# Kernel optimization log

Hardware: AMD Instinct MI355X
Metric: run time of the kernel (lower is better)

The kernel has to match this reference:

```python
import jax, jax.numpy as jnp
import numpy as np

N = 20000   # nodes
E = 40000   # directed edges
F_IN = 13   # dataset.num_features
G = 1000    # graphs in batch
DIMS = [(13, 32), (32, 64), (64, 64)]  # (M_in, M_out) per NNConv layer


def setup_inputs() -> dict:
    key = jax.random.key(0)
    ks = list(jax.random.split(key, 32))
    inp = {}
    inp["x"] = jax.random.normal(ks[0], (N, F_IN), jnp.float32)
    inp["edge_index"] = jax.random.randint(ks[1], (2, E), 0, N, dtype=jnp.int32)
    inp["edge_attr"] = jax.random.uniform(ks[2], (E, 5), dtype=jnp.float32)
    inp["batch"] = jnp.sort(jax.random.randint(ks[3], (N,), 0, G, dtype=jnp.int32))
    i = 4
    for l, (mi, mo) in enumerate(DIMS):
        inp[f"w1_{l}"] = jax.random.normal(ks[i], (5, 128), jnp.float32) / np.sqrt(5.0).astype(np.float32); i += 1
        inp[f"b1_{l}"] = jnp.zeros((128,), jnp.float32)
        inp[f"w2_{l}"] = jax.random.normal(ks[i], (128, mi * mo), jnp.float32) / np.sqrt(128.0).astype(np.float32); i += 1
        inp[f"b2_{l}"] = jnp.zeros((mi * mo,), jnp.float32)
        inp[f"root_{l}"] = jax.random.normal(ks[i], (mi, mo), jnp.float32) / np.sqrt(float(mi)).astype(np.float32); i += 1
        inp[f"bias_{l}"] = jnp.zeros((mo,), jnp.float32)
    inp["fc1_w"] = jax.random.normal(ks[i], (64, 32), jnp.float32) / 8.0; i += 1
    inp["fc1_b"] = jnp.zeros((32,), jnp.float32)
    inp["fc2_w"] = jax.random.normal(ks[i], (32, 16), jnp.float32) / np.sqrt(32.0).astype(np.float32); i += 1
    inp["fc2_b"] = jnp.zeros((16,), jnp.float32)
    inp["fc3_w"] = jax.random.normal(ks[i], (16, 1), jnp.float32) / 4.0; i += 1
    inp["fc3_b"] = jnp.zeros((1,), jnp.float32)
    return inp


def _nnconv(x, src, dst, edge_attr, w1, b1, w2, b2, root, bias, mi, mo):
    # edge MLP: [E,5] -> [E,128] -> [E, mi*mo] per-edge weight matrices
    h = jax.nn.relu(edge_attr @ w1 + b1)
    We = (h @ w2 + b2).reshape(-1, mi, mo)          # [E, mi, mo]
    msg = jnp.einsum('ei,eio->eo', x[src], We)      # gather + per-edge matmul
    agg = jax.ops.segment_sum(msg, dst, num_segments=x.shape[0])  # scatter-add
    return x @ root + agg + bias                    # NNConv root weight + bias


def _forward(x, edge_index, edge_attr, batch, convs, fc1_w, fc1_b, fc2_w, fc2_b, fc3_w, fc3_b):
    src, dst = edge_index[0], edge_index[1]
    for (mi, mo), (w1, b1, w2, b2, root, bias) in zip(DIMS, convs):
        x = jax.nn.elu(_nnconv(x, src, dst, edge_attr, w1, b1, w2, b2, root, bias, mi, mo))
    # scatter_mean pooling over graphs
    sums = jax.ops.segment_sum(x, batch, num_segments=G)
    cnt = jax.ops.segment_sum(jnp.ones((x.shape[0],), x.dtype), batch, num_segments=G)
    xg = sums / jnp.maximum(cnt, 1.0)[:, None]
    xg = jax.nn.elu(xg @ fc1_w + fc1_b)
    xg = jax.nn.elu(xg @ fc2_w + fc2_b)
    return (xg @ fc3_w + fc3_b).reshape(-1)


def reference(x, edge_index, edge_attr, batch,
              w1_0, b1_0, w2_0, b2_0, root_0, bias_0,
              w1_1, b1_1, w2_1, b2_1, root_1, bias_1,
              w1_2, b1_2, w2_2, b2_2, root_2, bias_2,
              fc1_w, fc1_b, fc2_w, fc2_b, fc3_w, fc3_b):
    convs = [(w1_0, b1_0, w2_0, b2_0, root_0, bias_0),
             (w1_1, b1_1, w2_1, b2_1, root_1, bias_1),
             (w1_2, b1_2, w2_2, b2_2, root_2, bias_2)]
    return _forward(x, edge_index, edge_attr, batch, convs,
                    fc1_w, fc1_b, fc2_w, fc2_b, fc3_w, fc3_b)
```

## Files before the change

kernel.cpp:

```cpp
#include <hip/hip_runtime.h>
#include <stdint.h>
#include <math.h>

typedef _Float16 half8_t __attribute__((ext_vector_type(8)));
typedef float floatx4 __attribute__((ext_vector_type(4)));

#define NN 20000
#define NE 40000
#define NG 1000
#define NBLK 157
#define NSPLIT 4

__global__ __launch_bounds__(256) void prep_all_kernel(
    const float* __restrict__ w2a, const float* __restrict__ b2a, _Float16* __restrict__ oa,
    const float* __restrict__ w2b, const float* __restrict__ b2b, _Float16* __restrict__ ob,
    const float* __restrict__ w2c, const float* __restrict__ b2c, _Float16* __restrict__ oc)
{
  const int TOT0 = 68 * 2 * 64, TOT1 = 132 * 4 * 64, TOT2 = 264 * 4 * 64;
  int idx = blockIdx.x * 256 + threadIdx.x;
  const float *w2, *b2; _Float16* op; int mi, mo, mpsh, CT;
  if (idx < TOT0) { w2 = w2a; b2 = b2a; op = oa; mi = 13; mo = 32; mpsh = 4; CT = 2; }
  else if (idx < TOT0 + TOT1) { idx -= TOT0; w2 = w2b; b2 = b2b; op = ob; mi = 32; mo = 64; mpsh = 5; CT = 4; }
  else if (idx < TOT0 + TOT1 + TOT2) { idx -= TOT0 + TOT1; w2 = w2c; b2 = b2c; op = oc; mi = 64; mo = 64; mpsh = 6; CT = 4; }
  else return;
  int l = idx & 63;
  int ct = (idx >> 6) % CT;
  int c = idx / (64 * CT);
  int q = l >> 4;
  int n = ct * 16 + (l & 15);
  int mask = (1 << mpsh) - 1;
  half8_t v;
#pragma unroll
  for (int j = 0; j < 8; ++j) {
    int r = c * 32 + q * 8 + j;
    int k = r >> mpsh, i = r & mask;
    float f = 0.f;
    if (i < mi) {
      if (k < 128) f = w2[(size_t)(k * mi + i) * mo + n];
      else if (k == 128) f = b2[(size_t)i * mo + n];
    }
    v[j] = (_Float16)f;
  }
  *(half8_t*)(op + (size_t)idx * 8) = v;
}

__global__ __launch_bounds__(256) void prep0_kernel(
    const float* __restrict__ x, const float* __restrict__ root,
    const float* __restrict__ bias, _Float16* __restrict__ e16,
    float* __restrict__ xn0)
{
  __shared__ float xs[8 * 13];
  int n0 = blockIdx.x * 8;
  int t = threadIdx.x;
  if (t < 104) xs[t] = x[(size_t)n0 * 13 + t];
  __syncthreads();
  if (t < 128) {
    int r = t >> 4, i = t & 15;
    e16[(size_t)(n0 + r) * 16 + i] = (i < 13) ? (_Float16)xs[r * 13 + i] : (_Float16)0.f;
  }
  int r = t >> 5, o = t & 31;
  float acc = bias[o];
#pragma unroll
  for (int i = 0; i < 13; ++i) acc = fmaf(xs[r * 13 + i], root[i * 32 + o], acc);
  xn0[(size_t)(n0 + r) * 32 + o] = acc;
}

template <int MI, int MOX>
__global__ __launch_bounds__(256) void elu_root_kernel(
    const float* __restrict__ xin, const float* __restrict__ root,
    const float* __restrict__ bias, _Float16* __restrict__ e16,
    float* __restrict__ xnext)
{
  constexpr int R = 256 / MOX;
  __shared__ float es[R * MI];
  int n0 = blockIdx.x * R;
  int t = threadIdx.x;
  for (int idx = t; idx < R * MI; idx += 256) {
    float v = xin[(size_t)n0 * MI + idx];
    v = v > 0.f ? v : (expf(v) - 1.f);
    es[idx] = v;
    e16[(size_t)n0 * MI + idx] = (_Float16)v;
  }
  __syncthreads();
  int r = t / MOX, o = t % MOX;
  float acc = bias[o];
#pragma unroll 8
  for (int i = 0; i < MI; ++i) acc = fmaf(es[r * MI + i], root[i * MOX + o], acc);
  xnext[(size_t)(n0 + r) * MOX + o] = acc;
}

template <int MIP, int MO, int NCC, int KCNT>
__global__ __launch_bounds__(256, 2) void msg5_kernel(
    const float* __restrict__ ea, const float* __restrict__ w1,
    const float* __restrict__ b1, const _Float16* __restrict__ xe,
    const int* __restrict__ src, const int* __restrict__ dst,
    const _Float16* __restrict__ w2h, float* __restrict__ xn)
{
  constexpr int CT = MO / 16;
  constexpr int CHB = CT * 1024;
  constexpr int XLSS = MIP + 8;
  constexpr int HST = 66;
  constexpr int SM = (XLSS > HST) ? XLSS : HST;
  constexpr int XV = (MIP == 64) ? 2 : 1;
  constexpr int NU = MIP / 8;

  __shared__ _Float16 sbuf[256 * SM];
  __shared__ uint4 wsb[2][CT * 64];
  __shared__ float w1s[5 * 128 + 128];
  __shared__ int dsts[256];

  const int t = threadIdx.x;
  const int wave = t >> 6, lane = t & 63;
  const int l15 = lane & 15, q = lane >> 4;
  const int split = blockIdx.x / NBLK;
  const int eblk = blockIdx.x % NBLK;
  const int e0 = eblk * 256;
  const int c0 = NCC * split;
  const int kg0 = KCNT * split;

  int eg = e0 + t; if (eg >= NE) eg = NE - 1;
  dsts[t] = dst[eg];
  float ear[5];
#pragma unroll
  for (int j = 0; j < 5; ++j) ear[j] = ea[(size_t)eg * 5 + j];
  {
    const uint4* xr = (const uint4*)(xe + (size_t)src[eg] * MIP);
    uint4* xd = (uint4*)(sbuf + t * XLSS);
#pragma unroll
    for (int u = 0; u < NU; ++u) xd[u] = xr[u];
  }
  for (int i = t; i < 768; i += 256) w1s[i] = (i < 640) ? w1[i] : b1[i - 640];
  __syncthreads();

  const int wbase = wave * 64;
  half8_t xf[4][XV];
#pragma unroll
  for (int s = 0; s < 4; ++s) {
    int el = wbase + s * 16 + l15;
    int i0 = (MIP == 16) ? (q & 1) * 8 : q * 8;
    xf[s][0] = *(const half8_t*)(sbuf + el * XLSS + i0);
    if constexpr (MIP == 64)
      xf[s][XV - 1] = *(const half8_t*)(sbuf + el * XLSS + 32 + q * 8);
  }
  __syncthreads();

#pragma unroll 4
  for (int kl = 0; kl < KCNT; ++kl) {
    int kg = kg0 + kl;
    float v;
    if (kg < 128) {
      v = w1s[640 + kg];
#pragma unroll
      for (int j = 0; j < 5; ++j) v = fmaf(ear[j], w1s[j * 128 + kg], v);
      v = fmaxf(v, 0.f);
    } else v = (kg == 128) ? 1.f : 0.f;
    sbuf[t * HST + kl] = (_Float16)v;
  }
  __syncthreads();

  floatx4 acc[4][CT];
#pragma unroll
  for (int s = 0; s < 4; ++s)
#pragma unroll
    for (int b = 0; b < CT; ++b) acc[s][b] = (floatx4){0.f, 0.f, 0.f, 0.f};

  const char* wgp = (const char*)w2h + (size_t)c0 * CHB;
  uint4 r4; uint2 r2;
  if constexpr (CT == 4) r4 = *(const uint4*)(wgp + t * 16);
  else r2 = *(const uint2*)(wgp + t * 8);

#pragma unroll 2
  for (int cc = 0; cc < NCC; ++cc) {
    if constexpr (CT == 4) wsb[cc & 1][t] = r4;
    else ((uint2*)wsb[cc & 1])[t] = r2;
    __syncthreads();
    if (cc + 1 < NCC) {
      if constexpr (CT == 4) r4 = *(const uint4*)(wgp + (size_t)(cc + 1) * CHB + t * 16);
      else r2 = *(const uint2*)(wgp + (size_t)(cc + 1) * CHB + t * 8);
    }
    const _Float16* wb = (const _Float16*)wsb[cc & 1];
    half8_t bf[CT];
#pragma unroll
    for (int b = 0; b < CT; ++b)
      bf[b] = *(const half8_t*)(wb + (b * 64 + lane) * 8);
    int kl;
    if constexpr (MIP == 64) kl = cc >> 1;
    else if constexpr (MIP == 32) kl = cc;
    else kl = 2 * cc + (q >> 1);
#pragma unroll
    for (int s = 0; s < 4; ++s) {
      _Float16 hv = sbuf[(wbase + s * 16 + l15) * HST + kl];
      half8_t af;
      if constexpr (MIP == 64) af = xf[s][cc & 1] * hv;
      else af = xf[s][0] * hv;
#pragma unroll
      for (int b = 0; b < CT; ++b)
        acc[s][b] = __builtin_amdgcn_mfma_f32_16x16x32_f16(af, bf[b], acc[s][b], 0, 0, 0);
    }
  }

#pragma unroll
  for (int s = 0; s < 4; ++s) {
    int rowb = wbase + s * 16 + q * 4;
#pragma unroll
    for (int b = 0; b < CT; ++b) {
      int n = b * 16 + l15;
#pragma unroll
      for (int r = 0; r < 4; ++r) {
        int row = rowb + r;
        if (e0 + row < NE)
          atomicAdd(&xn[(size_t)dsts[row] * MO + n], acc[s][b][r]);
      }
    }
  }
}

__global__ __launch_bounds__(64) void pool_fc_kernel(
    const float* __restrict__ xn2, const int* __restrict__ batch,
    const float* __restrict__ f1w, const float* __restrict__ f1b,
    const float* __restrict__ f2w, const float* __restrict__ f2b,
    const float* __restrict__ f3w, const float* __restrict__ f3b,
    float* __restrict__ out)
{
  __shared__ float xg[64]; __shared__ float a1[32]; __shared__ float a2[16];
  int g = blockIdx.x, t = threadIdx.x;
  int lo = 0, hi = NN;
  while (lo < hi) { int m = (lo + hi) >> 1; if (batch[m] < g) lo = m + 1; else hi = m; }
  int start = lo; hi = NN;
  while (lo < hi) { int m = (lo + hi) >> 1; if (batch[m] <= g) lo = m + 1; else hi = m; }
  int end = lo;
  float acc = 0.f;
  for (int n = start; n < end; ++n) {
    float v = xn2[(size_t)n * 64 + t];
    acc += v > 0.f ? v : (expf(v) - 1.f);
  }
  float c = (end > start) ? (float)(end - start) : 1.f;
  xg[t] = acc / c;
  __syncthreads();
  if (t < 32) {
    float a = f1b[t];
    for (int i = 0; i < 64; ++i) a = fmaf(xg[i], f1w[i * 32 + t], a);
    a1[t] = a > 0.f ? a : (expf(a) - 1.f);
  }
  __syncthreads();
  if (t < 16) {
    float a = f2b[t];
    for (int i = 0; i < 32; ++i) a = fmaf(a1[i], f2w[i * 16 + t], a);
    a2[t] = a > 0.f ? a : (expf(a) - 1.f);
  }
  __syncthreads();
  if (t == 0) {
    float a = f3b[0];
    for (int i = 0; i < 16; ++i) a = fmaf(a2[i], f3w[i], a);
    out[g] = a;
  }
}

extern "C" void kernel_launch(void* const* d_in, const int* in_sizes, int n_in,
                              void* d_out, int out_size, void* d_ws, size_t ws_size,
                              hipStream_t stream)
{
  const float* x_in  = (const float*)d_in[0];
  const int*   ei    = (const int*)d_in[1];
  const float* ea    = (const float*)d_in[2];
  const int*   batch = (const int*)d_in[3];
  const float* W1[3] = {(const float*)d_in[4],  (const float*)d_in[10], (const float*)d_in[16]};
  const float* B1[3] = {(const float*)d_in[5],  (const float*)d_in[11], (const float*)d_in[17]};
  const float* W2[3] = {(const float*)d_in[6],  (const float*)d_in[12], (const float*)d_in[18]};
  const float* B2[3] = {(const float*)d_in[7],  (const float*)d_in[13], (const float*)d_in[19]};
  const float* RT[3] = {(const float*)d_in[8],  (const float*)d_in[14], (const float*)d_in[20]};
  const float* BS[3] = {(const float*)d_in[9],  (const float*)d_in[15], (const float*)d_in[21]};
  const float* f1w = (const float*)d_in[22]; const float* f1b = (const float*)d_in[23];
  const float* f2w = (const float*)d_in[24]; const float* f2b = (const float*)d_in[25];
  const float* f3w = (const float*)d_in[26]; const float* f3b = (const float*)d_in[27];

  char* ws = (char*)d_ws;
  size_t off = 0;
  auto alloc = [&](size_t bytes) { void* p = ws + off; off += (bytes + 255) & ~(size_t)255; return p; };
  float*    xn0   = (float*)alloc((size_t)NN * 32 * 4);
  float*    xn1   = (float*)alloc((size_t)NN * 64 * 4);
  float*    xn2   = (float*)alloc((size_t)NN * 64 * 4);
  _Float16* e16_0 = (_Float16*)alloc((size_t)NN * 16 * 2);
  _Float16* e16_1 = (_Float16*)alloc((size_t)NN * 32 * 2);
  _Float16* e16_2 = (_Float16*)alloc((size_t)NN * 64 * 2);
  _Float16* w2h0  = (_Float16*)alloc((size_t)68 * 2048);
  _Float16* w2h1  = (_Float16*)alloc((size_t)132 * 4096);
  _Float16* w2h2  = (_Float16*)alloc((size_t)264 * 4096);

  const int* srcp = ei;
  const int* dstp = ei + NE;

  prep_all_kernel<<<(68*2*64 + 132*4*64 + 264*4*64 + 255) / 256, 256, 0, stream>>>(
      W2[0], B2[0], w2h0, W2[1], B2[1], w2h1, W2[2], B2[2], w2h2);
  prep0_kernel<<<NN / 8, 256, 0, stream>>>(x_in, RT[0], BS[0], e16_0, xn0);

  msg5_kernel<16, 32, 17, 34><<<NBLK * NSPLIT, 256, 0, stream>>>(
      ea, W1[0], B1[0], e16_0, srcp, dstp, w2h0, xn0);
  elu_root_kernel<32, 64><<<NN / 4, 256, 0, stream>>>(xn0, RT[1], BS[1], e16_1, xn1);

  msg5_kernel<32, 64, 33, 33><<<NBLK * NSPLIT, 256, 0, stream>>>(
      ea, W1[1], B1[1], e16_1, srcp, dstp, w2h1, xn1);
  elu_root_kernel<64, 64><<<NN / 4, 256, 0, stream>>>(xn1, RT[2], BS[2], e16_2, xn2);

  msg5_kernel<64, 64, 66, 33><<<NBLK * NSPLIT, 256, 0, stream>>>(
      ea, W1[2], B1[2], e16_2, srcp, dstp, w2h2, xn2);

  pool_fc_kernel<<<NG, 64, 0, stream>>>(xn2, batch, f1w, f1b, f2w, f2b, f3w, f3b, (float*)d_out);
}
```

Baseline: 319.1 us.

## Load MFMA B-fragments directly from global into a register ring, drop LDS staging

```diff
diff --git a/kernel.cpp b/kernel.cpp
--- a/kernel.cpp
+++ b/kernel.cpp
@@ -16,7 +16,7 @@
     const float* __restrict__ w2b, const float* __restrict__ b2b, _Float16* __restrict__ ob,
     const float* __restrict__ w2c, const float* __restrict__ b2c, _Float16* __restrict__ oc)
 {
-  const int TOT0 = 68 * 2 * 64, TOT1 = 132 * 4 * 64, TOT2 = 264 * 4 * 64;
+  const int TOT0 = 72 * 2 * 64, TOT1 = 132 * 4 * 64, TOT2 = 264 * 4 * 64;
   int idx = blockIdx.x * 256 + threadIdx.x;
   const float *w2, *b2; _Float16* op; int mi, mo, mpsh, CT;
   if (idx < TOT0) { w2 = w2a; b2 = b2a; op = oa; mi = 13; mo = 32; mpsh = 4; CT = 2; }
@@ -90,7 +90,7 @@
 }
 
 template <int MIP, int MO, int NCC, int KCNT>
-__global__ __launch_bounds__(256, 2) void msg5_kernel(
+__global__ __launch_bounds__(256, 2) void msg6_kernel(
     const float* __restrict__ ea, const float* __restrict__ w1,
     const float* __restrict__ b1, const _Float16* __restrict__ xe,
     const int* __restrict__ src, const int* __restrict__ dst,
@@ -99,13 +99,14 @@
   constexpr int CT = MO / 16;
   constexpr int CHB = CT * 1024;
   constexpr int XLSS = MIP + 8;
-  constexpr int HST = 66;
+  constexpr int HST = (KCNT + 2) & ~1;
   constexpr int SM = (XLSS > HST) ? XLSS : HST;
   constexpr int XV = (MIP == 64) ? 2 : 1;
   constexpr int NU = MIP / 8;
+  constexpr int MAC = (MIP == 64) ? 6 : 3;
+  constexpr int NMAC = NCC / MAC;
 
   __shared__ _Float16 sbuf[256 * SM];
-  __shared__ uint4 wsb[2][CT * 64];
   __shared__ float w1s[5 * 128 + 128];
   __shared__ int dsts[256];
 
@@ -164,38 +165,38 @@
 #pragma unroll
     for (int b = 0; b < CT; ++b) acc[s][b] = (floatx4){0.f, 0.f, 0.f, 0.f};
 
-  const char* wgp = (const char*)w2h + (size_t)c0 * CHB;
-  uint4 r4; uint2 r2;
-  if constexpr (CT == 4) r4 = *(const uint4*)(wgp + t * 16);
-  else r2 = *(const uint2*)(wgp + t * 8);
-
-#pragma unroll 2
-  for (int cc = 0; cc < NCC; ++cc) {
-    if constexpr (CT == 4) wsb[cc & 1][t] = r4;
-    else ((uint2*)wsb[cc & 1])[t] = r2;
-    __syncthreads();
-    if (cc + 1 < NCC) {
-      if constexpr (CT == 4) r4 = *(const uint4*)(wgp + (size_t)(cc + 1) * CHB + t * 16);
-      else r2 = *(const uint2*)(wgp + (size_t)(cc + 1) * CHB + t * 8);
-    }
-    const _Float16* wb = (const _Float16*)wsb[cc & 1];
-    half8_t bf[CT];
+  const char* wgp = (const char*)w2h + (size_t)c0 * CHB + (size_t)lane * 16;
+  half8_t bq[3][CT];
+#pragma unroll
+  for (int p = 0; p < 3; ++p)
 #pragma unroll
     for (int b = 0; b < CT; ++b)
-      bf[b] = *(const half8_t*)(wb + (b * 64 + lane) * 8);
-    int kl;
-    if constexpr (MIP == 64) kl = cc >> 1;
-    else if constexpr (MIP == 32) kl = cc;
-    else kl = 2 * cc + (q >> 1);
-#pragma unroll
-    for (int s = 0; s < 4; ++s) {
-      _Float16 hv = sbuf[(wbase + s * 16 + l15) * HST + kl];
-      half8_t af;
-      if constexpr (MIP == 64) af = xf[s][cc & 1] * hv;
-      else af = xf[s][0] * hv;
+      bq[p][b] = *(const half8_t*)(wgp + (size_t)p * CHB + b * 1024);
+
+  for (int m = 0; m < NMAC; ++m) {
+#pragma unroll
+    for (int j = 0; j < MAC; ++j) {
+      constexpr_hint:;
+      const int slot = j % 3;
+      const int cc = m * MAC + j;
+      int kl;
+      if constexpr (MIP == 64) kl = cc >> 1;
+      else if constexpr (MIP == 32) kl = cc;
+      else kl = 2 * cc + (q >> 1);
+#pragma unroll
+      for (int s = 0; s < 4; ++s) {
+        _Float16 hv = sbuf[(wbase + s * 16 + l15) * HST + kl];
+        half8_t af;
+        if constexpr (MIP == 64) af = xf[s][j & 1] * hv;
+        else af = xf[s][0] * hv;
+#pragma unroll
+        for (int b = 0; b < CT; ++b)
+          acc[s][b] = __builtin_amdgcn_mfma_f32_16x16x32_f16(af, bq[slot][b], acc[s][b], 0, 0, 0);
+      }
+      int cp = cc + 3; if (cp > NCC - 1) cp = NCC - 1;
 #pragma unroll
       for (int b = 0; b < CT; ++b)
-        acc[s][b] = __builtin_amdgcn_mfma_f32_16x16x32_f16(af, bf[b], acc[s][b], 0, 0, 0);
+        bq[slot][b] = *(const half8_t*)(wgp + (size_t)cp * CHB + b * 1024);
     }
   }
 
@@ -283,26 +284,26 @@
   _Float16* e16_0 = (_Float16*)alloc((size_t)NN * 16 * 2);
   _Float16* e16_1 = (_Float16*)alloc((size_t)NN * 32 * 2);
   _Float16* e16_2 = (_Float16*)alloc((size_t)NN * 64 * 2);
-  _Float16* w2h0  = (_Float16*)alloc((size_t)68 * 2048);
+  _Float16* w2h0  = (_Float16*)alloc((size_t)72 * 2048);
   _Float16* w2h1  = (_Float16*)alloc((size_t)132 * 4096);
   _Float16* w2h2  = (_Float16*)alloc((size_t)264 * 4096);
 
   const int* srcp = ei;
   const int* dstp = ei + NE;
 
-  prep_all_kernel<<<(68*2*64 + 132*4*64 + 264*4*64 + 255) / 256, 256, 0, stream>>>(
+  prep_all_kernel<<<(72*2*64 + 132*4*64 + 264*4*64 + 255) / 256, 256, 0, stream>>>(
       W2[0], B2[0], w2h0, W2[1], B2[1], w2h1, W2[2], B2[2], w2h2);
   prep0_kernel<<<NN / 8, 256, 0, stream>>>(x_in, RT[0], BS[0], e16_0, xn0);
 
-  msg5_kernel<16, 32, 17, 34><<<NBLK * NSPLIT, 256, 0, stream>>>(
+  msg6_kernel<16, 32, 18, 36><<<NBLK * NSPLIT, 256, 0, stream>>>(
       ea, W1[0], B1[0], e16_0, srcp, dstp, w2h0, xn0);
   elu_root_kernel<32, 64><<<NN / 4, 256, 0, stream>>>(xn0, RT[1], BS[1], e16_1, xn1);
 
-  msg5_kernel<32, 64, 33, 33><<<NBLK * NSPLIT, 256, 0, stream>>>(
+  msg6_kernel<32, 64, 33, 33><<<NBLK * NSPLIT, 256, 0, stream>>>(
       ea, W1[1], B1[1], e16_1, srcp, dstp, w2h1, xn1);
   elu_root_kernel<64, 64><<<NN / 4, 256, 0, stream>>>(xn1, RT[2], BS[2], e16_2, xn2);
 
-  msg5_kernel<64, 64, 66, 33><<<NBLK * NSPLIT, 256, 0, stream>>>(
+  msg6_kernel<64, 64, 66, 33><<<NBLK * NSPLIT, 256, 0, stream>>>(
       ea, W1[2], B1[2], e16_2, srcp, dstp, w2h2, xn2);
 
   pool_fc_kernel<<<NG, 64, 0, stream>>>(xn2, batch, f1w, f1b, f2w, f2b, f3w, f3b, (float*)d_out);
```

After: 313.8 us. Within noise of the previous version (-1.7%).

## Halve edges per block in message kernel to raise occupancy

Applied to the files above, without the earlier changes.

```diff
diff --git a/kernel.cpp b/kernel.cpp
--- a/kernel.cpp
+++ b/kernel.cpp
@@ -8,7 +8,7 @@
 #define NN 20000
 #define NE 40000
 #define NG 1000
-#define NBLK 157
+#define NBLK 313
 #define NSPLIT 4
 
 __global__ __launch_bounds__(256) void prep_all_kernel(
@@ -90,7 +90,7 @@
 }
 
 template <int MIP, int MO, int NCC, int KCNT>
-__global__ __launch_bounds__(256, 2) void msg5_kernel(
+__global__ __launch_bounds__(256, 4) void msg7_kernel(
     const float* __restrict__ ea, const float* __restrict__ w1,
     const float* __restrict__ b1, const _Float16* __restrict__ xe,
     const int* __restrict__ src, const int* __restrict__ dst,
@@ -99,68 +99,86 @@
   constexpr int CT = MO / 16;
   constexpr int CHB = CT * 1024;
   constexpr int XLSS = MIP + 8;
-  constexpr int HST = 66;
-  constexpr int SM = (XLSS > HST) ? XLSS : HST;
+  constexpr int HSTW = KCNT | 1;
   constexpr int XV = (MIP == 64) ? 2 : 1;
-  constexpr int NU = MIP / 8;
-
-  __shared__ _Float16 sbuf[256 * SM];
-  __shared__ uint4 wsb[2][CT * 64];
+  constexpr int NU2 = MIP / 16;
+  constexpr int KH = (KCNT + 1) >> 1;
+  constexpr int XB = 128 * XLSS * 2;
+  constexpr int HB = 128 * HSTW * 4;
+  constexpr int SBYTES = (XB > HB) ? XB : HB;
+
+  __shared__ char sb[SBYTES];
+  __shared__ uint4 wsb[2][CHB / 16];
   __shared__ float w1s[5 * 128 + 128];
-  __shared__ int dsts[256];
+  __shared__ int dsts[128];
+
+  _Float16* sxb = (_Float16*)sb;
+  unsigned* hls = (unsigned*)sb;
 
   const int t = threadIdx.x;
   const int wave = t >> 6, lane = t & 63;
   const int l15 = lane & 15, q = lane >> 4;
   const int split = blockIdx.x / NBLK;
-  const int eblk = blockIdx.x % NBLK;
-  const int e0 = eblk * 256;
+  const int e0 = (blockIdx.x % NBLK) * 128;
   const int c0 = NCC * split;
   const int kg0 = KCNT * split;
 
-  int eg = e0 + t; if (eg >= NE) eg = NE - 1;
-  dsts[t] = dst[eg];
+  {
+    int rowA = t >> 1;
+    int egA = e0 + rowA; if (egA >= NE) egA = NE - 1;
+    const uint4* xr = (const uint4*)(xe + (size_t)src[egA] * MIP);
+    uint4* xd = (uint4*)(sxb + rowA * XLSS);
+#pragma unroll
+    for (int u = 0; u < NU2; ++u) xd[(t & 1) * NU2 + u] = xr[(t & 1) * NU2 + u];
+  }
+  if (t < 128) {
+    int eg = e0 + t; if (eg >= NE) eg = NE - 1;
+    dsts[t] = dst[eg];
+  }
+  const int te = t & 127;
   float ear[5];
-#pragma unroll
-  for (int j = 0; j < 5; ++j) ear[j] = ea[(size_t)eg * 5 + j];
   {
-    const uint4* xr = (const uint4*)(xe + (size_t)src[eg] * MIP);
-    uint4* xd = (uint4*)(sbuf + t * XLSS);
-#pragma unroll
-    for (int u = 0; u < NU; ++u) xd[u] = xr[u];
+    int ege = e0 + te; if (ege >= NE) ege = NE - 1;
+#pragma unroll
+    for (int j = 0; j < 5; ++j) ear[j] = ea[(size_t)ege * 5 + j];
   }
   for (int i = t; i < 768; i += 256) w1s[i] = (i < 640) ? w1[i] : b1[i - 640];
   __syncthreads();
 
-  const int wbase = wave * 64;
-  half8_t xf[4][XV];
-#pragma unroll
-  for (int s = 0; s < 4; ++s) {
+  const int wbase = wave * 32;
+  half8_t xf[2][XV];
+#pragma unroll
+  for (int s = 0; s < 2; ++s) {
     int el = wbase + s * 16 + l15;
     int i0 = (MIP == 16) ? (q & 1) * 8 : q * 8;
-    xf[s][0] = *(const half8_t*)(sbuf + el * XLSS + i0);
+    xf[s][0] = *(const half8_t*)(sxb + el * XLSS + i0);
     if constexpr (MIP == 64)
-      xf[s][XV - 1] = *(const half8_t*)(sbuf + el * XLSS + 32 + q * 8);
-  }
-  __syncthreads();
-
-#pragma unroll 4
-  for (int kl = 0; kl < KCNT; ++kl) {
-    int kg = kg0 + kl;
-    float v;
-    if (kg < 128) {
-      v = w1s[640 + kg];
-#pragma unroll
-      for (int j = 0; j < 5; ++j) v = fmaf(ear[j], w1s[j * 128 + kg], v);
-      v = fmaxf(v, 0.f);
-    } else v = (kg == 128) ? 1.f : 0.f;
-    sbuf[t * HST + kl] = (_Float16)v;
-  }
-  __syncthreads();
-
-  floatx4 acc[4][CT];
-#pragma unroll
-  for (int s = 0; s < 4; ++s)
+      xf[s][XV - 1] = *(const half8_t*)(sxb + el * XLSS + 32 + q * 8);
+  }
+  __syncthreads();
+
+  {
+    int kh = t >> 7;
+    int klo = kh * KH;
+    int khi = klo + KH; if (khi > KCNT) khi = KCNT;
+    for (int kl = klo; kl < khi; ++kl) {
+      int kg = kg0 + kl;
+      float v;
+      if (kg < 128) {
+        v = w1s[640 + kg];
+#pragma unroll
+        for (int j = 0; j < 5; ++j) v = fmaf(ear[j], w1s[j * 128 + kg], v);
+        v = fmaxf(v, 0.f);
+      } else v = (kg == 128) ? 1.f : 0.f;
+      union { _Float16 f; unsigned short u; } cv; cv.f = (_Float16)v;
+      hls[te * HSTW + kl] = (unsigned)cv.u * 0x10001u;
+    }
+  }
+  __syncthreads();
+
+  floatx4 acc[2][CT];
+#pragma unroll
+  for (int s = 0; s < 2; ++s)
 #pragma unroll
     for (int b = 0; b < CT; ++b) acc[s][b] = (floatx4){0.f, 0.f, 0.f, 0.f};
 
@@ -188,8 +206,8 @@
     else if constexpr (MIP == 32) kl = cc;
     else kl = 2 * cc + (q >> 1);
 #pragma unroll
-    for (int s = 0; s < 4; ++s) {
-      _Float16 hv = sbuf[(wbase + s * 16 + l15) * HST + kl];
+    for (int s = 0; s < 2; ++s) {
+      _Float16 hv = *(const _Float16*)(hls + (wbase + s * 16 + l15) * HSTW + kl);
       half8_t af;
       if constexpr (MIP == 64) af = xf[s][cc & 1] * hv;
       else af = xf[s][0] * hv;
@@ -200,7 +218,7 @@
   }
 
 #pragma unroll
-  for (int s = 0; s < 4; ++s) {
+  for (int s = 0; s < 2; ++s) {
     int rowb = wbase + s * 16 + q * 4;
 #pragma unroll
     for (int b = 0; b < CT; ++b) {
@@ -294,15 +312,15 @@
       W2[0], B2[0], w2h0, W2[1], B2[1], w2h1, W2[2], B2[2], w2h2);
   prep0_kernel<<<NN / 8, 256, 0, stream>>>(x_in, RT[0], BS[0], e16_0, xn0);
 
-  msg5_kernel<16, 32, 17, 34><<<NBLK * NSPLIT, 256, 0, stream>>>(
+  msg7_kernel<16, 32, 17, 34><<<NBLK * NSPLIT, 256, 0, stream>>>(
       ea, W1[0], B1[0], e16_0, srcp, dstp, w2h0, xn0);
   elu_root_kernel<32, 64><<<NN / 4, 256, 0, stream>>>(xn0, RT[1], BS[1], e16_1, xn1);
 
-  msg5_kernel<32, 64, 33, 33><<<NBLK * NSPLIT, 256, 0, stream>>>(
+  msg7_kernel<32, 64, 33, 33><<<NBLK * NSPLIT, 256, 0, stream>>>(
       ea, W1[1], B1[1], e16_1, srcp, dstp, w2h1, xn1);
   elu_root_kernel<64, 64><<<NN / 4, 256, 0, stream>>>(xn1, RT[2], BS[2], e16_2, xn2);
 
-  msg5_kernel<64, 64, 66, 33><<<NBLK * NSPLIT, 256, 0, stream>>>(
+  msg7_kernel<64, 64, 66, 33><<<NBLK * NSPLIT, 256, 0, stream>>>(
       ea, W1[2], B1[2], e16_2, srcp, dstp, w2h2, xn2);
 
   pool_fc_kernel<<<NG, 64, 0, stream>>>(xn2, batch, f1w, f1b, f2w, f2b, f3w, f3b, (float*)d_out);
```

Result: faster. 305.0 us (-4.4%).
